# Performance work log

Hardware: AMD Instinct MI355X
Metric: run time of the kernel (lower is better)

The kernel has to match this reference:

```python
import jax, jax.numpy as jnp
import numpy as np

D_MODEL = 1024
OUTPUT_DIM = 1024
NUM_HEADS = 16
HEAD_DIM = D_MODEL // NUM_HEADS


def _xavier(key, shape):
    fan_in, fan_out = shape[1], shape[0]
    limit = float(np.sqrt(6.0 / (fan_in + fan_out)))
    return jax.random.uniform(key, shape, jnp.float32, -limit, limit)


def setup_inputs() -> dict:
    key = jax.random.key(0)
    k_h, k_q, k_k, k_o = jax.random.split(key, 4)
    H = jax.random.normal(k_h, (2, 2048, D_MODEL), dtype=jnp.float32)
    # nn.Linear weights are [out, in]; xavier_uniform on weights, default (uniform) biases left as zeros-equivalent
    Wq = _xavier(k_q, (D_MODEL, D_MODEL))
    bq = jnp.zeros((D_MODEL,), jnp.float32)
    Wk = _xavier(k_k, (D_MODEL, D_MODEL))
    bk = jnp.zeros((D_MODEL,), jnp.float32)
    Wo = _xavier(k_o, (OUTPUT_DIM, D_MODEL))
    bo = jnp.zeros((OUTPUT_DIM,), jnp.float32)
    return {"H": H, "Wq": Wq, "bq": bq, "Wk": Wk, "bk": bk, "Wo": Wo, "bo": bo}


def reference(H, Wq, bq, Wk, bk, Wo, bo):
    B, S, _ = H.shape
    Q = H @ Wq.T + bq  # [B,S,D]
    K = H @ Wk.T + bk
    # split heads -> [B,nh,S,hd]
    Qh = Q.reshape(B, S, NUM_HEADS, HEAD_DIM).transpose(0, 2, 1, 3)
    Kh = K.reshape(B, S, NUM_HEADS, HEAD_DIM).transpose(0, 2, 1, 3)
    Vh = H.reshape(B, S, NUM_HEADS, HEAD_DIM).transpose(0, 2, 1, 3)
    scale = 1.0 / jnp.sqrt(jnp.float32(HEAD_DIM))
    A = jnp.einsum('bhqd,bhkd->bhqk', Qh, Kh) * scale  # [B,nh,S,S]
    A = jax.nn.softmax(A, axis=-1)
    out = jnp.einsum('bhqk,bhkd->bhqd', A, Vh)  # [B,nh,S,hd]
    out = out.transpose(0, 2, 1, 3).reshape(B, S, D_MODEL)
    return out @ Wo.T + bo
```

## Files before the change

kernel.cpp:

```cpp
#include <hip/hip_runtime.h>
#include <stdint.h>

#define BB 2
#define SS 2048
#define DD 1024
#define NH 16
#define HD 64
#define MM 4096

typedef __bf16 bf16x8 __attribute__((ext_vector_type(8)));
typedef __bf16 bf16x4 __attribute__((ext_vector_type(4)));
typedef float  f32x4  __attribute__((ext_vector_type(4)));

__device__ __forceinline__ unsigned short f2bf(float f) {
    __bf16 h = (__bf16)f;
    return __builtin_bit_cast(unsigned short, h);
}

__device__ __forceinline__ void async_cp16(const void* g, const void* l) {
    __builtin_amdgcn_global_load_lds(
        (const __attribute__((address_space(1))) void*)(uintptr_t)g,
        (__attribute__((address_space(3))) void*)(uint32_t)(uintptr_t)l,
        16, 0, 0);
}

__device__ __forceinline__ f32x4 mfma16(bf16x8 a, bf16x8 b, f32x4 c) {
    return __builtin_amdgcn_mfma_f32_16x16x32_bf16(a, b, c, 0, 0, 0);
}

__global__ __launch_bounds__(256) void k_cvtw(const float* __restrict__ Wq,
                                              const float* __restrict__ Wk,
                                              const float* __restrict__ Wo,
                                              unsigned short* __restrict__ Wqb,
                                              unsigned short* __restrict__ Wkb,
                                              unsigned short* __restrict__ Wob) {
    int g = blockIdx.x;
    const float* src; unsigned short* dst; int base;
    if (g < 512)       { src = Wq; dst = Wqb; base = g; }
    else if (g < 1024) { src = Wk; dst = Wkb; base = g - 512; }
    else               { src = Wo; dst = Wob; base = g - 1024; }
    int i = (base * 256 + threadIdx.x) * 8;
    float4 a = *(const float4*)(src + i);
    float4 b = *(const float4*)(src + i + 4);
    unsigned short o[8];
    o[0] = f2bf(a.x); o[1] = f2bf(a.y); o[2] = f2bf(a.z); o[3] = f2bf(a.w);
    o[4] = f2bf(b.x); o[5] = f2bf(b.y); o[6] = f2bf(b.z); o[7] = f2bf(b.w);
    *(ulonglong2*)(dst + i) = *(ulonglong2*)o;
}

__global__ __launch_bounds__(256) void k_prep(const float* __restrict__ H,
                                              unsigned short* __restrict__ Hb,
                                              unsigned short* __restrict__ Vt) {
    __shared__ float tile[128][68];
    const int sb = blockIdx.x, h = blockIdx.y, b = blockIdx.z;
    const int t = threadIdx.x;
    const int col4 = t & 15;
    const int srow0 = t >> 4;
#pragma unroll
    for (int p = 0; p < 8; ++p) {
        int s = p * 16 + srow0;
        float4 v = *(const float4*)(H + (size_t)(b * SS + sb * 128 + s) * DD + h * HD + col4 * 4);
        *(float4*)&tile[s][col4 * 4] = v;
    }
    __syncthreads();
#pragma unroll
    for (int it = 0; it < 4; ++it) {
        int task = it * 256 + t;
        int s = task >> 3;
        int dg = task & 7;
        unsigned short pk[8];
#pragma unroll
        for (int j = 0; j < 8; ++j) pk[j] = f2bf(tile[s][dg * 8 + j]);
        *(ulonglong2*)(Hb + (size_t)(b * SS + sb * 128 + s) * DD + h * HD + dg * 8) = *(ulonglong2*)pk;
    }
#pragma unroll
    for (int it = 0; it < 4; ++it) {
        int task = it * 256 + t;
        int d = task >> 4;
        int sg = task & 15;
        unsigned short pk[8];
#pragma unroll
        for (int j = 0; j < 8; ++j) pk[j] = f2bf(tile[sg * 8 + j][d]);
        *(ulonglong2*)(Vt + (size_t)((b * NH + h) * HD + d) * SS + sb * 128 + sg * 8) = *(ulonglong2*)pk;
    }
}

template <int TM, bool BF16OUT>
__device__ __forceinline__ void gemm_body(const unsigned short* __restrict__ A,
                                          const unsigned short* __restrict__ Bt,
                                          const float* __restrict__ bias,
                                          void* __restrict__ Cp, float oscale) {
    constexpr int MT = TM / 32;
    constexpr int AR = (TM * 4) / 256;
    __shared__ unsigned short lsA[2][TM * 32];
    __shared__ unsigned short lsB[2][128 * 32];
    const int tid = threadIdx.x;
    const int lane = tid & 63;
    const int w = tid >> 6;
    const int wm = w & 1, wn = w >> 1;
    const int r = lane & 15, quad = lane >> 4;
    const int mBase = blockIdx.y * TM;
    const int nBase = blockIdx.x * 128;

    const unsigned short* gA[AR]; uint laOff[AR];
#pragma unroll
    for (int t = 0; t < AR; ++t) {
        int l = t * 256 + tid;
        int c = l ^ ((l >> 3) & 7);
        int row = c >> 2, kc = c & 3;
        gA[t] = A + (size_t)(mBase + row) * 1024 + kc * 8;
        laOff[t] = l * 8;
    }
    const unsigned short* gB[2]; uint lbOff[2];
#pragma unroll
    for (int t = 0; t < 2; ++t) {
        int l = t * 256 + tid;
        int c = l ^ ((l >> 3) & 7);
        int row = c >> 2, kc = c & 3;
        gB[t] = Bt + (size_t)(nBase + row) * 1024 + kc * 8;
        lbOff[t] = l * 8;
    }
    uint aOff[MT], bOff[4];
#pragma unroll
    for (int mt = 0; mt < MT; ++mt) {
        int rowA = wm * (TM / 2) + mt * 16 + r;
        int c = rowA * 4 + quad;
        aOff[mt] = (uint)((c ^ ((c >> 3) & 7)) * 8);
    }
#pragma unroll
    for (int nt = 0; nt < 4; ++nt) {
        int rowB = wn * 64 + nt * 16 + r;
        int c = rowB * 4 + quad;
        bOff[nt] = (uint)((c ^ ((c >> 3) & 7)) * 8);
    }

    f32x4 acc[MT][4];
#pragma unroll
    for (int i = 0; i < MT; ++i)
#pragma unroll
        for (int j = 0; j < 4; ++j) acc[i][j] = f32x4{0.f, 0.f, 0.f, 0.f};

    auto stage = [&](int buf) {
#pragma unroll
        for (int t = 0; t < AR; ++t) { async_cp16(gA[t], &lsA[buf][laOff[t]]); gA[t] += 32; }
#pragma unroll
        for (int t = 0; t < 2; ++t)  { async_cp16(gB[t], &lsB[buf][lbOff[t]]); gB[t] += 32; }
    };

    stage(0);
    for (int kb = 0; kb < 32; ++kb) {
        const int cur = kb & 1;
        __syncthreads();
        if (kb + 1 < 32) stage(cur ^ 1);

        bf16x8 af[MT], bf[4];
#pragma unroll
        for (int mt = 0; mt < MT; ++mt) af[mt] = *(const bf16x8*)&lsA[cur][aOff[mt]];
#pragma unroll
        for (int nt = 0; nt < 4; ++nt)  bf[nt] = *(const bf16x8*)&lsB[cur][bOff[nt]];
#pragma unroll
        for (int mt = 0; mt < MT; ++mt)
#pragma unroll
            for (int nt = 0; nt < 4; ++nt)
                acc[mt][nt] = mfma16(af[mt], bf[nt], acc[mt][nt]);
    }

    float bv[4];
#pragma unroll
    for (int nt = 0; nt < 4; ++nt) bv[nt] = bias[nBase + wn * 64 + nt * 16 + r];
#pragma unroll
    for (int mt = 0; mt < MT; ++mt)
#pragma unroll
        for (int nt = 0; nt < 4; ++nt) {
            int colg = nBase + wn * 64 + nt * 16 + r;
#pragma unroll
            for (int reg = 0; reg < 4; ++reg) {
                int rowg = mBase + wm * (TM / 2) + mt * 16 + quad * 4 + reg;
                float v = (acc[mt][nt][reg] + bv[nt]) * oscale;
                if (BF16OUT)
                    ((unsigned short*)Cp)[(size_t)rowg * 1024 + colg] = f2bf(v);
                else
                    ((float*)Cp)[(size_t)rowg * 1024 + colg] = v;
            }
        }
}

#define QSCALE 0.1803368801111137f

__global__ __launch_bounds__(256) void k_gemm_qk(const unsigned short* __restrict__ Hb,
                                                 const unsigned short* __restrict__ Wqb,
                                                 const unsigned short* __restrict__ Wkb,
                                                 const float* __restrict__ bq,
                                                 const float* __restrict__ bk,
                                                 unsigned short* __restrict__ Q,
                                                 unsigned short* __restrict__ K) {
    const unsigned short* Bt = blockIdx.z ? Wkb : Wqb;
    const float* bias = blockIdx.z ? bk : bq;
    unsigned short* C = blockIdx.z ? K : Q;
    float os = blockIdx.z ? 1.0f : QSCALE;
    gemm_body<64, true>(Hb, Bt, bias, C, os);
}

__global__ __launch_bounds__(256) void k_gemm_out(const unsigned short* __restrict__ Ctx,
                                                  const unsigned short* __restrict__ Wob,
                                                  const float* __restrict__ bo,
                                                  float* __restrict__ Out) {
    gemm_body<64, false>(Ctx, Wob, bo, Out, 1.0f);
}

__global__ __launch_bounds__(256) void k_attn(const unsigned short* __restrict__ Q,
                                              const unsigned short* __restrict__ K,
                                              const unsigned short* __restrict__ Vt,
                                              unsigned short* __restrict__ Ctx) {
    __shared__ unsigned short lsK[2][64 * 64];
    __shared__ unsigned short lsV[2][64 * 64];
    __shared__ unsigned short lsP[4 * 16 * 64];
    const int tid = threadIdx.x;
    const int lane = tid & 63;
    const int w = tid >> 6;
    const int r = lane & 15, quad = lane >> 4;
    const int qb = blockIdx.x, h = blockIdx.y, b = blockIdx.z;

    const int qrow = qb * 64 + w * 16 + r;
    const size_t qoff = (size_t)(b * SS + qrow) * DD + h * HD;
    bf16x8 aq[2];
    aq[0] = *(const bf16x8*)(Q + qoff + quad * 8);
    aq[1] = *(const bf16x8*)(Q + qoff + 32 + quad * 8);

    f32x4 accO[4];
#pragma unroll
    for (int nt = 0; nt < 4; ++nt) accO[nt] = f32x4{0.f, 0.f, 0.f, 0.f};
    float lsum[4] = {0.f, 0.f, 0.f, 0.f};

    const unsigned short* gK[2]; const unsigned short* gV[2]; uint lO[2];
#pragma unroll
    for (int t = 0; t < 2; ++t) {
        int l = t * 256 + tid;
        int c = l ^ ((l >> 3) & 7);
        int row = c >> 3, kc = c & 7;
        int srow = 4 * (row & 15) + (row >> 4);
        gK[t] = K + (size_t)(b * SS + srow) * DD + h * HD + kc * 8;
        gV[t] = Vt + (size_t)((b * NH + h) * HD + row) * SS + kc * 8;
        lO[t] = l * 8;
    }
    uint off[2][4];
#pragma unroll
    for (int t = 0; t < 2; ++t)
#pragma unroll
        for (int nt = 0; nt < 4; ++nt) {
            int rowX = nt * 16 + r;
            int c = rowX * 8 + t * 4 + quad;
            off[t][nt] = (uint)((c ^ ((c >> 3) & 7)) * 8);
        }
    uint pw[4], pr[2];
#pragma unroll
    for (int reg = 0; reg < 4; ++reg) {
        int prow = quad * 4 + reg;
        pw[reg] = (uint)(prow * 64 + ((r >> 1) ^ (prow & 7)) * 8 + (r & 1) * 4);
    }
#pragma unroll
    for (int t = 0; t < 2; ++t)
        pr[t] = (uint)(r * 64 + ((4 * t + quad) ^ (r & 7)) * 8);
    unsigned short* Pw = lsP + w * 1024;

    auto stage = [&](int buf) {
#pragma unroll
        for (int t = 0; t < 2; ++t) {
            async_cp16(gK[t], &lsK[buf][lO[t]]); gK[t] += 64 * DD;
            async_cp16(gV[t], &lsV[buf][lO[t]]); gV[t] += 64;
        }
    };

    stage(0);
    for (int kt = 0; kt < 32; ++kt) {
        const int cur = kt & 1;
        __syncthreads();
        if (kt + 1 < 32) stage(cur ^ 1);

        f32x4 s[4];
#pragma unroll
        for (int nt = 0; nt < 4; ++nt) s[nt] = f32x4{0.f, 0.f, 0.f, 0.f};
#pragma unroll
        for (int t = 0; t < 2; ++t)
#pragma unroll
            for (int nt = 0; nt < 4; ++nt)
                s[nt] = mfma16(aq[t], *(const bf16x8*)&lsK[cur][off[t][nt]], s[nt]);

#pragma unroll
        for (int reg = 0; reg < 4; ++reg) {
            float p0 = __builtin_amdgcn_exp2f(s[0][reg]);
            float p1 = __builtin_amdgcn_exp2f(s[1][reg]);
            float p2 = __builtin_amdgcn_exp2f(s[2][reg]);
            float p3 = __builtin_amdgcn_exp2f(s[3][reg]);
            lsum[reg] += (p0 + p1) + (p2 + p3);
            bf16x4 pk = {(__bf16)p0, (__bf16)p1, (__bf16)p2, (__bf16)p3};
            *(bf16x4*)&Pw[pw[reg]] = pk;
        }

#pragma unroll
        for (int t = 0; t < 2; ++t) {
            bf16x8 ap = *(const bf16x8*)&Pw[pr[t]];
#pragma unroll
            for (int nt = 0; nt < 4; ++nt)
                accO[nt] = mfma16(ap, *(const bf16x8*)&lsV[cur][off[t][nt]], accO[nt]);
        }
    }

    float linv[4];
#pragma unroll
    for (int reg = 0; reg < 4; ++reg) {
        float l = lsum[reg];
        l += __shfl_xor(l, 1);
        l += __shfl_xor(l, 2);
        l += __shfl_xor(l, 4);
        l += __shfl_xor(l, 8);
        linv[reg] = 1.0f / l;
    }
#pragma unroll
    for (int nt = 0; nt < 4; ++nt) {
        int d = nt * 16 + r;
#pragma unroll
        for (int reg = 0; reg < 4; ++reg) {
            int qr = qb * 64 + w * 16 + quad * 4 + reg;
            Ctx[(size_t)(b * SS + qr) * DD + h * HD + d] = f2bf(accO[nt][reg] * linv[reg]);
        }
    }
}

extern "C" void kernel_launch(void* const* d_in, const int* in_sizes, int n_in,
                              void* d_out, int out_size, void* d_ws, size_t ws_size,
                              hipStream_t stream) {
    (void)in_sizes; (void)n_in; (void)out_size; (void)ws_size;
    const float* H  = (const float*)d_in[0];
    const float* Wq = (const float*)d_in[1];
    const float* bq = (const float*)d_in[2];
    const float* Wk = (const float*)d_in[3];
    const float* bk = (const float*)d_in[4];
    const float* Wo = (const float*)d_in[5];
    const float* bo = (const float*)d_in[6];
    float* Out = (float*)d_out;

    char* ws = (char*)d_ws;
    unsigned short* Hb  = (unsigned short*)(ws);
    unsigned short* Qb  = (unsigned short*)(ws + 8388608);
    unsigned short* Kb  = (unsigned short*)(ws + 16777216);
    unsigned short* Ctx = (unsigned short*)(ws + 25165824);
    unsigned short* Vt  = (unsigned short*)(ws + 33554432);
    unsigned short* Wqb = (unsigned short*)(ws + 41943040);
    unsigned short* Wkb = (unsigned short*)(ws + 44040192);
    unsigned short* Wob = (unsigned short*)(ws + 46137344);

    k_cvtw<<<dim3(1536), dim3(256), 0, stream>>>(Wq, Wk, Wo, Wqb, Wkb, Wob);
    k_prep<<<dim3(16, NH, BB), dim3(256), 0, stream>>>(H, Hb, Vt);
    k_gemm_qk<<<dim3(8, 64, 2), dim3(256), 0, stream>>>(Hb, Wqb, Wkb, bq, bk, Qb, Kb);
    k_attn<<<dim3(32, NH, BB), dim3(256), 0, stream>>>(Qb, Kb, Vt, Ctx);
    k_gemm_out<<<dim3(8, 64, 1), dim3(256), 0, stream>>>(Ctx, Wob, bo, Out);
}
```

Before: 201.8 us.

## Double query rows per attention block, merge prep kernels, enlarge QK GEMM tile

The attention kernel now handles 128 query rows per block, 32 per wave in two sub-tiles. Each K/V fragment read from LDS feeds two MFMAs, which halves K/V staging traffic per query and halves the grid. The weight-conversion and H-prep kernels are merged into one launch to save a kernel launch. The QK projection GEMM uses a 128-row tile with half the M-blocks. The cost is more registers and LDS per block, which may reduce occupancy, and fewer blocks to spread across CUs.

```diff
diff --git a/kernel.cpp b/kernel.cpp
--- a/kernel.cpp
+++ b/kernel.cpp
@@ -28,32 +28,34 @@
     return __builtin_amdgcn_mfma_f32_16x16x32_bf16(a, b, c, 0, 0, 0);
 }
 
-__global__ __launch_bounds__(256) void k_cvtw(const float* __restrict__ Wq,
+__global__ __launch_bounds__(256) void k_prep(const float* __restrict__ H,
+                                              const float* __restrict__ Wq,
                                               const float* __restrict__ Wk,
                                               const float* __restrict__ Wo,
+                                              unsigned short* __restrict__ Hb,
+                                              unsigned short* __restrict__ Vt,
                                               unsigned short* __restrict__ Wqb,
                                               unsigned short* __restrict__ Wkb,
                                               unsigned short* __restrict__ Wob) {
-    int g = blockIdx.x;
-    const float* src; unsigned short* dst; int base;
-    if (g < 512)       { src = Wq; dst = Wqb; base = g; }
-    else if (g < 1024) { src = Wk; dst = Wkb; base = g - 512; }
-    else               { src = Wo; dst = Wob; base = g - 1024; }
-    int i = (base * 256 + threadIdx.x) * 8;
-    float4 a = *(const float4*)(src + i);
-    float4 b = *(const float4*)(src + i + 4);
-    unsigned short o[8];
-    o[0] = f2bf(a.x); o[1] = f2bf(a.y); o[2] = f2bf(a.z); o[3] = f2bf(a.w);
-    o[4] = f2bf(b.x); o[5] = f2bf(b.y); o[6] = f2bf(b.z); o[7] = f2bf(b.w);
-    *(ulonglong2*)(dst + i) = *(ulonglong2*)o;
-}
-
-__global__ __launch_bounds__(256) void k_prep(const float* __restrict__ H,
-                                              unsigned short* __restrict__ Hb,
-                                              unsigned short* __restrict__ Vt) {
     __shared__ float tile[128][68];
-    const int sb = blockIdx.x, h = blockIdx.y, b = blockIdx.z;
+    const int bx = blockIdx.x;
     const int t = threadIdx.x;
+    if (bx >= 512) {
+        int g = bx - 512;
+        const float* src; unsigned short* dst; int base;
+        if (g < 512)       { src = Wq; dst = Wqb; base = g; }
+        else if (g < 1024) { src = Wk; dst = Wkb; base = g - 512; }
+        else               { src = Wo; dst = Wob; base = g - 1024; }
+        int i = (base * 256 + t) * 8;
+        float4 a = *(const float4*)(src + i);
+        float4 b = *(const float4*)(src + i + 4);
+        unsigned short o[8];
+        o[0] = f2bf(a.x); o[1] = f2bf(a.y); o[2] = f2bf(a.z); o[3] = f2bf(a.w);
+        o[4] = f2bf(b.x); o[5] = f2bf(b.y); o[6] = f2bf(b.z); o[7] = f2bf(b.w);
+        *(ulonglong2*)(dst + i) = *(ulonglong2*)o;
+        return;
+    }
+    const int sb = bx & 15, h = (bx >> 4) & 15, b = bx >> 8;
     const int col4 = t & 15;
     const int srow0 = t >> 4;
 #pragma unroll
@@ -198,7 +200,7 @@
     const float* bias = blockIdx.z ? bk : bq;
     unsigned short* C = blockIdx.z ? K : Q;
     float os = blockIdx.z ? 1.0f : QSCALE;
-    gemm_body<64, true>(Hb, Bt, bias, C, os);
+    gemm_body<128, true>(Hb, Bt, bias, C, os);
 }
 
 __global__ __launch_bounds__(256) void k_gemm_out(const unsigned short* __restrict__ Ctx,
@@ -214,23 +216,28 @@
                                               unsigned short* __restrict__ Ctx) {
     __shared__ unsigned short lsK[2][64 * 64];
     __shared__ unsigned short lsV[2][64 * 64];
-    __shared__ unsigned short lsP[4 * 16 * 64];
+    __shared__ unsigned short lsP[4 * 32 * 64];
     const int tid = threadIdx.x;
     const int lane = tid & 63;
     const int w = tid >> 6;
     const int r = lane & 15, quad = lane >> 4;
     const int qb = blockIdx.x, h = blockIdx.y, b = blockIdx.z;
 
-    const int qrow = qb * 64 + w * 16 + r;
-    const size_t qoff = (size_t)(b * SS + qrow) * DD + h * HD;
-    bf16x8 aq[2];
-    aq[0] = *(const bf16x8*)(Q + qoff + quad * 8);
-    aq[1] = *(const bf16x8*)(Q + qoff + 32 + quad * 8);
-
-    f32x4 accO[4];
-#pragma unroll
-    for (int nt = 0; nt < 4; ++nt) accO[nt] = f32x4{0.f, 0.f, 0.f, 0.f};
-    float lsum[4] = {0.f, 0.f, 0.f, 0.f};
+    bf16x8 aq[2][2];
+#pragma unroll
+    for (int sub = 0; sub < 2; ++sub) {
+        const int qrow = qb * 128 + w * 32 + sub * 16 + r;
+        const size_t qoff = (size_t)(b * SS + qrow) * DD + h * HD;
+        aq[sub][0] = *(const bf16x8*)(Q + qoff + quad * 8);
+        aq[sub][1] = *(const bf16x8*)(Q + qoff + 32 + quad * 8);
+    }
+
+    f32x4 accO[2][4];
+#pragma unroll
+    for (int sub = 0; sub < 2; ++sub)
+#pragma unroll
+        for (int nt = 0; nt < 4; ++nt) accO[sub][nt] = f32x4{0.f, 0.f, 0.f, 0.f};
+    float lsum[2][4] = {{0.f, 0.f, 0.f, 0.f}, {0.f, 0.f, 0.f, 0.f}};
 
     const unsigned short* gK[2]; const unsigned short* gV[2]; uint lO[2];
 #pragma unroll
@@ -261,7 +268,7 @@
 #pragma unroll
     for (int t = 0; t < 2; ++t)
         pr[t] = (uint)(r * 64 + ((4 * t + quad) ^ (r & 7)) * 8);
-    unsigned short* Pw = lsP + w * 1024;
+    unsigned short* Pw = lsP + w * 2048;
 
     auto stage = [&](int buf) {
 #pragma unroll
@@ -277,52 +284,66 @@
         __syncthreads();
         if (kt + 1 < 32) stage(cur ^ 1);
 
-        f32x4 s[4];
-#pragma unroll
-        for (int nt = 0; nt < 4; ++nt) s[nt] = f32x4{0.f, 0.f, 0.f, 0.f};
+        f32x4 s[2][4];
+#pragma unroll
+        for (int sub = 0; sub < 2; ++sub)
+#pragma unroll
+            for (int nt = 0; nt < 4; ++nt) s[sub][nt] = f32x4{0.f, 0.f, 0.f, 0.f};
 #pragma unroll
         for (int t = 0; t < 2; ++t)
 #pragma unroll
-            for (int nt = 0; nt < 4; ++nt)
-                s[nt] = mfma16(aq[t], *(const bf16x8*)&lsK[cur][off[t][nt]], s[nt]);
-
+            for (int nt = 0; nt < 4; ++nt) {
+                bf16x8 bk = *(const bf16x8*)&lsK[cur][off[t][nt]];
+                s[0][nt] = mfma16(aq[0][t], bk, s[0][nt]);
+                s[1][nt] = mfma16(aq[1][t], bk, s[1][nt]);
+            }
+
+#pragma unroll
+        for (int sub = 0; sub < 2; ++sub)
+#pragma unroll
+            for (int reg = 0; reg < 4; ++reg) {
+                float p0 = __builtin_amdgcn_exp2f(s[sub][0][reg]);
+                float p1 = __builtin_amdgcn_exp2f(s[sub][1][reg]);
+                float p2 = __builtin_amdgcn_exp2f(s[sub][2][reg]);
+                float p3 = __builtin_amdgcn_exp2f(s[sub][3][reg]);
+                lsum[sub][reg] += (p0 + p1) + (p2 + p3);
+                bf16x4 pk = {(__bf16)p0, (__bf16)p1, (__bf16)p2, (__bf16)p3};
+                *(bf16x4*)&Pw[sub * 1024 + pw[reg]] = pk;
+            }
+
+#pragma unroll
+        for (int t = 0; t < 2; ++t) {
+            bf16x8 ap0 = *(const bf16x8*)&Pw[pr[t]];
+            bf16x8 ap1 = *(const bf16x8*)&Pw[1024 + pr[t]];
+#pragma unroll
+            for (int nt = 0; nt < 4; ++nt) {
+                bf16x8 bv = *(const bf16x8*)&lsV[cur][off[t][nt]];
+                accO[0][nt] = mfma16(ap0, bv, accO[0][nt]);
+                accO[1][nt] = mfma16(ap1, bv, accO[1][nt]);
+            }
+        }
+    }
+
+#pragma unroll
+    for (int sub = 0; sub < 2; ++sub) {
+        float linv[4];
 #pragma unroll
         for (int reg = 0; reg < 4; ++reg) {
-            float p0 = __builtin_amdgcn_exp2f(s[0][reg]);
-            float p1 = __builtin_amdgcn_exp2f(s[1][reg]);
-            float p2 = __builtin_amdgcn_exp2f(s[2][reg]);
-            float p3 = __builtin_amdgcn_exp2f(s[3][reg]);
-            lsum[reg] += (p0 + p1) + (p2 + p3);
-            bf16x4 pk = {(__bf16)p0, (__bf16)p1, (__bf16)p2, (__bf16)p3};
-            *(bf16x4*)&Pw[pw[reg]] = pk;
-        }
-
-#pragma unroll
-        for (int t = 0; t < 2; ++t) {
-            bf16x8 ap = *(const bf16x8*)&Pw[pr[t]];
-#pragma unroll
-            for (int nt = 0; nt < 4; ++nt)
-                accO[nt] = mfma16(ap, *(const bf16x8*)&lsV[cur][off[t][nt]], accO[nt]);
-        }
-    }
-
-    float linv[4];
-#pragma unroll
-    for (int reg = 0; reg < 4; ++reg) {
-        float l = lsum[reg];
-        l += __shfl_xor(l, 1);
-        l += __shfl_xor(l, 2);
-        l += __shfl_xor(l, 4);
-        l += __shfl_xor(l, 8);
-        linv[reg] = 1.0f / l;
-    }
-#pragma unroll
-    for (int nt = 0; nt < 4; ++nt) {
-        int d = nt * 16 + r;
-#pragma unroll
-        for (int reg = 0; reg < 4; ++reg) {
-            int qr = qb * 64 + w * 16 + quad * 4 + reg;
-            Ctx[(size_t)(b * SS + qr) * DD + h * HD + d] = f2bf(accO[nt][reg] * linv[reg]);
+            float l = lsum[sub][reg];
+            l += __shfl_xor(l, 1);
+            l += __shfl_xor(l, 2);
+            l += __shfl_xor(l, 4);
+            l += __shfl_xor(l, 8);
+            linv[reg] = 1.0f / l;
+        }
+#pragma unroll
+        for (int nt = 0; nt < 4; ++nt) {
+            int d = nt * 16 + r;
+#pragma unroll
+            for (int reg = 0; reg < 4; ++reg) {
+                int qr = qb * 128 + w * 32 + sub * 16 + quad * 4 + reg;
+                Ctx[(size_t)(b * SS + qr) * DD + h * HD + d] = f2bf(accO[sub][nt][reg] * linv[reg]);
+            }
         }
     }
 }
@@ -350,9 +371,8 @@
     unsigned short* Wkb = (unsigned short*)(ws + 44040192);
     unsigned short* Wob = (unsigned short*)(ws + 46137344);
 
-    k_cvtw<<<dim3(1536), dim3(256), 0, stream>>>(Wq, Wk, Wo, Wqb, Wkb, Wob);
-    k_prep<<<dim3(16, NH, BB), dim3(256), 0, stream>>>(H, Hb, Vt);
-    k_gemm_qk<<<dim3(8, 64, 2), dim3(256), 0, stream>>>(Hb, Wqb, Wkb, bq, bk, Qb, Kb);
-    k_attn<<<dim3(32, NH, BB), dim3(256), 0, stream>>>(Qb, Kb, Vt, Ctx);
+    k_prep<<<dim3(2048), dim3(256), 0, stream>>>(H, Wq, Wk, Wo, Hb, Vt, Wqb, Wkb, Wob);
+    k_gemm_qk<<<dim3(8, 32, 2), dim3(256), 0, stream>>>(Hb, Wqb, Wkb, bq, bk, Qb, Kb);
+    k_attn<<<dim3(16, NH, BB), dim3(256), 0, stream>>>(Qb, Kb, Vt, Ctx);
     k_gemm_out<<<dim3(8, 64, 1), dim3(256), 0, stream>>>(Ctx, Wob, bo, Out);
 }
```

New measurement: 181.3 us. 10.1% less time.
